# Optimization experiments

Measured on AMD Instinct MI355X. Metric: run time of the kernel, lower is better.

## Reference

```python
import jax, jax.numpy as jnp
import numpy as np

EPS = 0.01  # args.eps in the original code
N = 4194304
DIM = 3


def _neg_linear(x, W, b):
    # NegativeLinear weight reparameterization: forces effective weights negative
    Wr = jnp.where(W >= 0, -jnp.exp(-W - EPS), W - jnp.exp(-EPS))
    return x @ Wr.T + b


def setup_inputs() -> dict:
    key = jax.random.key(0)
    ks = jax.random.split(key, 12)
    d = {
        "x0": jax.random.normal(ks[0], (N, DIM), dtype=jnp.float32),
        "W_in": jax.random.normal(ks[1], (7, DIM), dtype=jnp.float32) * float(np.sqrt(2.0 / DIM)),
        "b_in": jnp.zeros((7,), jnp.float32),
        "W_out": jax.random.normal(ks[10], (1, 7), dtype=jnp.float32) * float(np.sqrt(2.0 / 7)),
        "b_out": jnp.zeros((1,), jnp.float32),
        "Wl_out": jax.random.normal(ks[11], (1, DIM), dtype=jnp.float32) * float(np.sqrt(2.0 / DIM)),
        "bl_out": jnp.zeros((1,), jnp.float32),
    }
    for i in range(4):
        d[f"Wp{i+1}"] = jax.random.normal(ks[2 + 2 * i], (7, 7), dtype=jnp.float32) * float(np.sqrt(2.0 / 7))
        d[f"bp{i+1}"] = jnp.zeros((7,), jnp.float32)
        d[f"Wl{i+1}"] = jax.random.normal(ks[3 + 2 * i], (7, DIM), dtype=jnp.float32) * float(np.sqrt(2.0 / DIM))
        d[f"bl{i+1}"] = jnp.zeros((7,), jnp.float32)
    return d


def reference(x0, W_in, b_in, Wp1, bp1, Wl1, bl1, Wp2, bp2, Wl2, bl2,
              Wp3, bp3, Wl3, bl3, Wp4, bp4, Wl4, bl4,
              W_out, b_out, Wl_out, bl_out):
    sp = jax.nn.softplus
    x = -sp(x0 @ W_in.T + b_in)
    x = -sp(_neg_linear(x, Wp1, bp1) + x0 @ Wl1.T + bl1)
    x = -sp(_neg_linear(x, Wp2, bp2) + x0 @ Wl2.T + bl2)
    x = -sp(_neg_linear(x, Wp3, bp3) + x0 @ Wl3.T + bl3)
    x = -sp(_neg_linear(x, Wp4, bp4) + x0 @ Wl4.T + bl4)
    S_out = -sp(_neg_linear(x, W_out, b_out) + x0 @ Wl_out.T + bl_out)
    return S_out  # [N, 1]
```

## Files before the change

kernel.cpp:

```cpp
#include <hip/hip_runtime.h>
#include <math.h>

#define NEG_EPS 0.01f
#define LOG2E 1.4426950408889634f
#define LN2   0.6931471805599453f
#define NW 404

typedef float f32x2 __attribute__((ext_vector_type(2)));

#if __has_builtin(__builtin_amdgcn_exp2f)
#define EXP2F(x) __builtin_amdgcn_exp2f(x)
#else
#define EXP2F(x) exp2f(x)
#endif
#if __has_builtin(__builtin_amdgcn_logf)
#define LOG2F(x) __builtin_amdgcn_logf(x)
#else
#define LOG2F(x) __log2f(x)
#endif

struct Params {
  const float* W_in;  const float* b_in;
  const float* W_out; const float* b_out;
  const float* Wl_out;const float* bl_out;
  const float* Wp[4]; const float* bp[4];
  const float* Wl[4]; const float* bl[4];
};

__device__ __forceinline__ float neg_rep_m(float v) {
  return (v >= 0.0f) ? expf(-v - NEG_EPS) : (expf(-NEG_EPS) - v);
}

__device__ __forceinline__ f32x2 pk_fma_lo(f32x2 w, f32x2 v, f32x2 c) {
  f32x2 d;
  asm("v_pk_fma_f32 %0, %1, %2, %3 op_sel:[0,0,0] op_sel_hi:[0,1,1]"
      : "=v"(d) : "v"(w), "v"(v), "v"(c));
  return d;
}
__device__ __forceinline__ f32x2 pk_fma_hi(f32x2 w, f32x2 v, f32x2 c) {
  f32x2 d;
  asm("v_pk_fma_f32 %0, %1, %2, %3 op_sel:[1,0,0] op_sel_hi:[1,1,1]"
      : "=v"(d) : "v"(w), "v"(v), "v"(c));
  return d;
}

__device__ __forceinline__ f32x2 H2f(f32x2 t) {
  f32x2 r;
  float ex = EXP2F(-fabsf(t.x));
  float ey = EXP2F(-fabsf(t.y));
  float lx = LOG2F(1.0f + ex);
  float ly = LOG2F(1.0f + ey);
  r.x = fmaxf(t.x, 0.0f) + lx;
  r.y = fmaxf(t.y, 0.0f) + ly;
  return r;
}

__device__ float fetch_w(int i, const Params& p) {
  if (i < 56) {
    int j = i >> 3, c_ = i & 7;
    if (c_ < 3) return LOG2E * p.W_in[j * 3 + c_];
    if (c_ == 4 || c_ == 5) return LOG2E * p.b_in[j];
    return 0.0f;
  }
  i -= 56;
  if (i < 336) {
    int L = i / 84, r = i % 84, j = r / 12, c_ = r % 12;
    if (c_ < 7)  return neg_rep_m(p.Wp[L][j * 7 + c_]);
    if (c_ < 10) return LOG2E * p.Wl[L][j * 3 + (c_ - 7)];
    return LOG2E * (p.bp[L][j] + p.bl[L][j]);
  }
  i -= 336;
  if (i < 7)  return neg_rep_m(p.W_out[i]);
  if (i < 10) return LOG2E * p.Wl_out[i - 7];
  return LOG2E * (p.b_out[0] + p.bl_out[0]);
}

__device__ __forceinline__ f32x2 dot10(f32x2 w0, f32x2 w1, f32x2 w2_,
                                       f32x2 w3, f32x2 w4_, f32x2 w5,
                                       const f32x2 (&H)[7], const f32x2 (&X)[3]) {
  f32x2 acc = w5;
  acc = pk_fma_lo(w0, H[0], acc);
  acc = pk_fma_hi(w0, H[1], acc);
  acc = pk_fma_lo(w1, H[2], acc);
  acc = pk_fma_hi(w1, H[3], acc);
  acc = pk_fma_lo(w2_, H[4], acc);
  acc = pk_fma_hi(w2_, H[5], acc);
  acc = pk_fma_lo(w3, H[6], acc);
  acc = pk_fma_hi(w3, X[0], acc);
  acc = pk_fma_lo(w4_, X[1], acc);
  acc = pk_fma_hi(w4_, X[2], acc);
  return acc;
}

__global__ __launch_bounds__(256) void entropy_fwd(
    const float4* __restrict__ x4, float4* __restrict__ out4,
    Params p, int nthreads) {
  __shared__ float wsm[NW];
  for (int i = threadIdx.x; i < NW; i += 256) wsm[i] = fetch_w(i, p);
  __syncthreads();
  const f32x2* w2 = (const f32x2*)wsm;

  int idx = blockIdx.x * 256 + threadIdx.x;
  if (idx >= nthreads) return;

  float4 a = x4[idx * 3 + 0];
  float4 b = x4[idx * 3 + 1];
  float4 c = x4[idx * 3 + 2];
  f32x2 Xa[3] = {{a.x, a.w}, {a.y, b.x}, {a.z, b.y}};
  f32x2 Xb[3] = {{b.z, c.y}, {b.w, c.z}, {c.x, c.w}};

  f32x2 Ha[7], Hb[7];

  #pragma unroll
  for (int j = 0; j < 7; ++j) {
    const f32x2* rec = w2 + 4 * j;
    f32x2 r0 = rec[0], r1 = rec[1], r2v = rec[2];
    f32x2 ta = r2v, tb = r2v;
    ta = pk_fma_lo(r0, Xa[0], ta);  tb = pk_fma_lo(r0, Xb[0], tb);
    ta = pk_fma_hi(r0, Xa[1], ta);  tb = pk_fma_hi(r0, Xb[1], tb);
    ta = pk_fma_lo(r1, Xa[2], ta);  tb = pk_fma_lo(r1, Xb[2], tb);
    Ha[j] = H2f(ta);
    Hb[j] = H2f(tb);
  }

  #pragma unroll
  for (int L = 0; L < 4; ++L) {
    const f32x2* base = w2 + 28 + 42 * L;
    f32x2 Na[7], Nb[7];
    #pragma unroll
    for (int j = 0; j < 7; ++j) {
      const f32x2* wp = base + 6 * j;
      f32x2 w0 = wp[0], w1 = wp[1], w2_ = wp[2], w3 = wp[3], w4_ = wp[4], w5 = wp[5];
      Na[j] = H2f(dot10(w0, w1, w2_, w3, w4_, w5, Ha, Xa));
      Nb[j] = H2f(dot10(w0, w1, w2_, w3, w4_, w5, Hb, Xb));
    }
    #pragma unroll
    for (int j = 0; j < 7; ++j) { Ha[j] = Na[j]; Hb[j] = Nb[j]; }
  }

  {
    const f32x2* wp = w2 + 196;
    f32x2 w0 = wp[0], w1 = wp[1], w2_ = wp[2], w3 = wp[3], w4_ = wp[4], w5 = wp[5];
    f32x2 HA = H2f(dot10(w0, w1, w2_, w3, w4_, w5, Ha, Xa));
    f32x2 HB = H2f(dot10(w0, w1, w2_, w3, w4_, w5, Hb, Xb));
    float4 o;
    o.x = -LN2 * HA.x;
    o.y = -LN2 * HA.y;
    o.z = -LN2 * HB.x;
    o.w = -LN2 * HB.y;
    out4[idx] = o;
  }
}

extern "C" void kernel_launch(void* const* d_in, const int* in_sizes, int n_in,
                              void* d_out, int out_size, void* d_ws, size_t ws_size,
                              hipStream_t stream) {
  (void)n_in; (void)d_ws; (void)ws_size;
  Params p;
  p.W_in   = (const float*)d_in[1];
  p.b_in   = (const float*)d_in[2];
  p.W_out  = (const float*)d_in[3];
  p.b_out  = (const float*)d_in[4];
  p.Wl_out = (const float*)d_in[5];
  p.bl_out = (const float*)d_in[6];
  for (int i = 0; i < 4; ++i) {
    p.Wp[i] = (const float*)d_in[7 + 4 * i];
    p.bp[i] = (const float*)d_in[8 + 4 * i];
    p.Wl[i] = (const float*)d_in[9 + 4 * i];
    p.bl[i] = (const float*)d_in[10 + 4 * i];
  }

  int n_rows   = in_sizes[0] / 3;
  int nthreads = (n_rows + 3) / 4;
  int blocks   = (nthreads + 255) / 256;

  entropy_fwd<<<blocks, 256, 0, stream>>>(
      (const float4*)d_in[0], (float4*)d_out, p, nthreads);
}
```

Measured before the change: 61.72 us.

## Stage transformed weights in workspace via prep kernel and load them into SGPRs

Adds a one-block prep kernel that computes the reparameterized, log2e-scaled weights once into the workspace buffer. The main kernel then reads them with scalar loads into SGPRs, with the packed FMA weight operand changed to an SGPR constraint. This removes the per-block shared-memory fill, its __syncthreads, and the LDS reads of weights in the inner loops. It adds a second kernel launch plus serialized s_waitcnt waits per layer, and the layer loop is no longer unrolled.

```diff
diff --git a/kernel.cpp b/kernel.cpp
--- a/kernel.cpp
+++ b/kernel.cpp
@@ -4,9 +4,12 @@
 #define NEG_EPS 0.01f
 #define LOG2E 1.4426950408889634f
 #define LN2   0.6931471805599453f
-#define NW 404
-
-typedef float f32x2 __attribute__((ext_vector_type(2)));
+#define NWS 390
+
+typedef float f32x2  __attribute__((ext_vector_type(2)));
+typedef float f32x4  __attribute__((ext_vector_type(4)));
+typedef float f32x8  __attribute__((ext_vector_type(8)));
+typedef float f32x16 __attribute__((ext_vector_type(16)));
 
 #if __has_builtin(__builtin_amdgcn_exp2f)
 #define EXP2F(x) __builtin_amdgcn_exp2f(x)
@@ -31,16 +34,41 @@
   return (v >= 0.0f) ? expf(-v - NEG_EPS) : (expf(-NEG_EPS) - v);
 }
 
+__device__ float fetch_staged(int i, const Params& p) {
+  if (i < 42) {
+    int j = i / 6, c = i % 6;
+    if (c < 3)  return LOG2E * p.W_in[j * 3 + c];
+    if (c == 3) return 0.0f;
+    return LOG2E * p.b_in[j];
+  }
+  i -= 42;
+  if (i < 336) {
+    int L = i / 84, r = i % 84, j = r / 12, c = r % 12;
+    if (c < 7)  return neg_rep_m(p.Wp[L][j * 7 + c]);
+    if (c < 10) return LOG2E * p.Wl[L][j * 3 + (c - 7)];
+    return LOG2E * (p.bp[L][j] + p.bl[L][j]);
+  }
+  i -= 336;
+  if (i < 7)  return neg_rep_m(p.W_out[i]);
+  if (i < 10) return LOG2E * p.Wl_out[i - 7];
+  return LOG2E * (p.b_out[0] + p.bl_out[0]);
+}
+
+__global__ void prep_weights(Params p, float* ws) {
+  int i = threadIdx.x;
+  if (i < NWS) ws[i] = fetch_staged(i, p);
+}
+
 __device__ __forceinline__ f32x2 pk_fma_lo(f32x2 w, f32x2 v, f32x2 c) {
   f32x2 d;
   asm("v_pk_fma_f32 %0, %1, %2, %3 op_sel:[0,0,0] op_sel_hi:[0,1,1]"
-      : "=v"(d) : "v"(w), "v"(v), "v"(c));
+      : "=v"(d) : "s"(w), "v"(v), "v"(c));
   return d;
 }
 __device__ __forceinline__ f32x2 pk_fma_hi(f32x2 w, f32x2 v, f32x2 c) {
   f32x2 d;
   asm("v_pk_fma_f32 %0, %1, %2, %3 op_sel:[1,0,0] op_sel_hi:[1,1,1]"
-      : "=v"(d) : "v"(w), "v"(v), "v"(c));
+      : "=v"(d) : "s"(w), "v"(v), "v"(c));
   return d;
 }
 
@@ -53,26 +81,6 @@
   r.x = fmaxf(t.x, 0.0f) + lx;
   r.y = fmaxf(t.y, 0.0f) + ly;
   return r;
-}
-
-__device__ float fetch_w(int i, const Params& p) {
-  if (i < 56) {
-    int j = i >> 3, c_ = i & 7;
-    if (c_ < 3) return LOG2E * p.W_in[j * 3 + c_];
-    if (c_ == 4 || c_ == 5) return LOG2E * p.b_in[j];
-    return 0.0f;
-  }
-  i -= 56;
-  if (i < 336) {
-    int L = i / 84, r = i % 84, j = r / 12, c_ = r % 12;
-    if (c_ < 7)  return neg_rep_m(p.Wp[L][j * 7 + c_]);
-    if (c_ < 10) return LOG2E * p.Wl[L][j * 3 + (c_ - 7)];
-    return LOG2E * (p.bp[L][j] + p.bl[L][j]);
-  }
-  i -= 336;
-  if (i < 7)  return neg_rep_m(p.W_out[i]);
-  if (i < 10) return LOG2E * p.Wl_out[i - 7];
-  return LOG2E * (p.b_out[0] + p.bl_out[0]);
 }
 
 __device__ __forceinline__ f32x2 dot10(f32x2 w0, f32x2 w1, f32x2 w2_,
@@ -92,14 +100,27 @@
   return acc;
 }
 
+__device__ __forceinline__ f32x2 pair_in(const f32x16& a, const f32x16& b,
+                                         const f32x8& c, const f32x2& d, int p) {
+  if (p < 8)  return (f32x2){a[2 * p], a[2 * p + 1]};
+  if (p < 16) { int q = 2 * (p - 8); return (f32x2){b[q], b[q + 1]}; }
+  if (p < 20) { int q = 2 * (p - 16); return (f32x2){c[q], c[q + 1]}; }
+  return d;
+}
+__device__ __forceinline__ f32x2 hpair(const f32x16& a0, const f32x16& a1,
+                                       const f32x16& a2, const f32x16& a3,
+                                       const f32x16& a4, const f32x4& a5, int p) {
+  if (p < 8)  return (f32x2){a0[2 * p], a0[2 * p + 1]};
+  if (p < 16) { int q = 2 * (p - 8);  return (f32x2){a1[q], a1[q + 1]}; }
+  if (p < 24) { int q = 2 * (p - 16); return (f32x2){a2[q], a2[q + 1]}; }
+  if (p < 32) { int q = 2 * (p - 24); return (f32x2){a3[q], a3[q + 1]}; }
+  if (p < 40) { int q = 2 * (p - 32); return (f32x2){a4[q], a4[q + 1]}; }
+  { int q = 2 * (p - 40); return (f32x2){a5[q], a5[q + 1]}; }
+}
+
 __global__ __launch_bounds__(256) void entropy_fwd(
     const float4* __restrict__ x4, float4* __restrict__ out4,
-    Params p, int nthreads) {
-  __shared__ float wsm[NW];
-  for (int i = threadIdx.x; i < NW; i += 256) wsm[i] = fetch_w(i, p);
-  __syncthreads();
-  const f32x2* w2 = (const f32x2*)wsm;
-
+    const float* __restrict__ ws, int nthreads) {
   int idx = blockIdx.x * 256 + threadIdx.x;
   if (idx >= nthreads) return;
 
@@ -111,36 +132,73 @@
 
   f32x2 Ha[7], Hb[7];
 
-  #pragma unroll
-  for (int j = 0; j < 7; ++j) {
-    const f32x2* rec = w2 + 4 * j;
-    f32x2 r0 = rec[0], r1 = rec[1], r2v = rec[2];
-    f32x2 ta = r2v, tb = r2v;
-    ta = pk_fma_lo(r0, Xa[0], ta);  tb = pk_fma_lo(r0, Xb[0], tb);
-    ta = pk_fma_hi(r0, Xa[1], ta);  tb = pk_fma_hi(r0, Xb[1], tb);
-    ta = pk_fma_lo(r1, Xa[2], ta);  tb = pk_fma_lo(r1, Xb[2], tb);
-    Ha[j] = H2f(ta);
-    Hb[j] = H2f(tb);
-  }
-
-  #pragma unroll
+  {
+    f32x16 t0, t1; f32x8 t2; f32x2 t3;
+    asm volatile(
+        "s_load_dwordx16 %0, %4, 0x0\n\t"
+        "s_load_dwordx16 %1, %4, 0x40\n\t"
+        "s_load_dwordx8  %2, %4, 0x80\n\t"
+        "s_load_dwordx2  %3, %4, 0xa0\n\t"
+        "s_waitcnt lgkmcnt(0)"
+        : "=&s"(t0), "=&s"(t1), "=&s"(t2), "=&s"(t3)
+        : "s"(ws));
+    #pragma unroll
+    for (int j = 0; j < 7; ++j) {
+      f32x2 p0 = pair_in(t0, t1, t2, t3, 3 * j + 0);
+      f32x2 p1 = pair_in(t0, t1, t2, t3, 3 * j + 1);
+      f32x2 p2 = pair_in(t0, t1, t2, t3, 3 * j + 2);
+      f32x2 ta = p2, tb = p2;
+      ta = pk_fma_lo(p0, Xa[0], ta);  tb = pk_fma_lo(p0, Xb[0], tb);
+      ta = pk_fma_hi(p0, Xa[1], ta);  tb = pk_fma_hi(p0, Xb[1], tb);
+      ta = pk_fma_lo(p1, Xa[2], ta);  tb = pk_fma_lo(p1, Xb[2], tb);
+      Ha[j] = H2f(ta);
+      Hb[j] = H2f(tb);
+    }
+  }
+
+  const float* lp = ws + 42;
+  #pragma unroll 1
   for (int L = 0; L < 4; ++L) {
-    const f32x2* base = w2 + 28 + 42 * L;
+    f32x16 a0, a1, a2, a3, a4; f32x4 a5;
+    asm volatile(
+        "s_load_dwordx16 %0, %6, 0x0\n\t"
+        "s_load_dwordx16 %1, %6, 0x40\n\t"
+        "s_load_dwordx16 %2, %6, 0x80\n\t"
+        "s_load_dwordx16 %3, %6, 0xc0\n\t"
+        "s_load_dwordx16 %4, %6, 0x100\n\t"
+        "s_load_dwordx4  %5, %6, 0x140\n\t"
+        "s_waitcnt lgkmcnt(0)"
+        : "=&s"(a0), "=&s"(a1), "=&s"(a2), "=&s"(a3), "=&s"(a4), "=&s"(a5)
+        : "s"(lp));
     f32x2 Na[7], Nb[7];
     #pragma unroll
     for (int j = 0; j < 7; ++j) {
-      const f32x2* wp = base + 6 * j;
-      f32x2 w0 = wp[0], w1 = wp[1], w2_ = wp[2], w3 = wp[3], w4_ = wp[4], w5 = wp[5];
+      const int P = 6 * j;
+      f32x2 w0  = hpair(a0, a1, a2, a3, a4, a5, P + 0);
+      f32x2 w1  = hpair(a0, a1, a2, a3, a4, a5, P + 1);
+      f32x2 w2_ = hpair(a0, a1, a2, a3, a4, a5, P + 2);
+      f32x2 w3  = hpair(a0, a1, a2, a3, a4, a5, P + 3);
+      f32x2 w4_ = hpair(a0, a1, a2, a3, a4, a5, P + 4);
+      f32x2 w5  = hpair(a0, a1, a2, a3, a4, a5, P + 5);
       Na[j] = H2f(dot10(w0, w1, w2_, w3, w4_, w5, Ha, Xa));
       Nb[j] = H2f(dot10(w0, w1, w2_, w3, w4_, w5, Hb, Xb));
     }
     #pragma unroll
     for (int j = 0; j < 7; ++j) { Ha[j] = Na[j]; Hb[j] = Nb[j]; }
+    lp += 84;
   }
 
   {
-    const f32x2* wp = w2 + 196;
-    f32x2 w0 = wp[0], w1 = wp[1], w2_ = wp[2], w3 = wp[3], w4_ = wp[4], w5 = wp[5];
+    f32x8 o0; f32x4 o1;
+    asm volatile(
+        "s_load_dwordx8 %0, %2, 0x0\n\t"
+        "s_load_dwordx4 %1, %2, 0x20\n\t"
+        "s_waitcnt lgkmcnt(0)"
+        : "=&s"(o0), "=&s"(o1)
+        : "s"(ws + 378));
+    f32x2 w0  = {o0[0], o0[1]}, w1 = {o0[2], o0[3]};
+    f32x2 w2_ = {o0[4], o0[5]}, w3 = {o0[6], o0[7]};
+    f32x2 w4_ = {o1[0], o1[1]}, w5 = {o1[2], o1[3]};
     f32x2 HA = H2f(dot10(w0, w1, w2_, w3, w4_, w5, Ha, Xa));
     f32x2 HB = H2f(dot10(w0, w1, w2_, w3, w4_, w5, Hb, Xb));
     float4 o;
@@ -155,7 +213,7 @@
 extern "C" void kernel_launch(void* const* d_in, const int* in_sizes, int n_in,
                               void* d_out, int out_size, void* d_ws, size_t ws_size,
                               hipStream_t stream) {
-  (void)n_in; (void)d_ws; (void)ws_size;
+  (void)n_in; (void)ws_size;
   Params p;
   p.W_in   = (const float*)d_in[1];
   p.b_in   = (const float*)d_in[2];
@@ -170,10 +228,12 @@
     p.bl[i] = (const float*)d_in[10 + 4 * i];
   }
 
+  float* ws = (float*)d_ws;
+  prep_weights<<<1, 512, 0, stream>>>(p, ws);
+
   int n_rows   = in_sizes[0] / 3;
   int nthreads = (n_rows + 3) / 4;
   int blocks   = (nthreads + 255) / 256;
-
   entropy_fwd<<<blocks, 256, 0, stream>>>(
-      (const float4*)d_in[0], (float4*)d_out, p, nthreads);
-}
+      (const float4*)d_in[0], (float4*)d_out, ws, nthreads);
+}
```

Result: slower. 63.86 us (+3.5%).
